# Kernel tuning notes

Measured on AMD Instinct MI355X. Metric: run time of the kernel, lower is better.

The kernel has to match this reference:

```python
import jax, jax.numpy as jnp
import numpy as np

N_MEL = 80; H = 512; HD = H // 2; R = 2; A = 128; NF = 32; K = 31
EMB = 512; ENC = 512; NSYM = 100


def _lstm_layer(x, lengths, Wih, Whh, b):
    # x: [B,T,D]; masked unidirectional LSTM (packed-sequence semantics:
    # state frozen and output zero past each sequence length).
    B, T, _ = x.shape
    Hh = Whh.shape[1]
    def step(carry, inp):
        h, c = carry
        xt, t = inp
        g = xt @ Wih.T + h @ Whh.T + b
        i, f, gg, o = jnp.split(g, 4, axis=-1)
        c_new = jax.nn.sigmoid(f) * c + jax.nn.sigmoid(i) * jnp.tanh(gg)
        h_new = jax.nn.sigmoid(o) * jnp.tanh(c_new)
        m = (t < lengths)[:, None]
        return (jnp.where(m, h_new, h), jnp.where(m, c_new, c)), jnp.where(m, h_new, 0.0)
    init = (jnp.zeros((B, Hh), x.dtype), jnp.zeros((B, Hh), x.dtype))
    _, ys = jax.lax.scan(step, init, (x.transpose(1, 0, 2), jnp.arange(T)))
    return ys.transpose(1, 0, 2)


def _bilstm(x, lengths, fw, bw):
    # bidirectional masked LSTM: backward dir runs on the sequence reversed
    # within its valid length (pack_padded_sequence semantics).
    T = x.shape[1]
    t = jnp.arange(T)
    idx = jnp.clip(lengths[:, None] - 1 - t[None, :], 0)
    x_rev = jnp.take_along_axis(x, idx[:, :, None], axis=1)
    out_f = _lstm_layer(x, lengths, *fw)
    out_r = _lstm_layer(x_rev, lengths, *bw)
    out_b = jnp.take_along_axis(out_r, idx[:, :, None], axis=1)
    out_b = jnp.where((t[None, :] < lengths[:, None])[:, :, None], out_b, 0.0)
    return jnp.concatenate([out_f, out_b], axis=-1)


def _forward(mel, mel_lengths, decoder_inputs, start_embedding,
             l1f_Wih, l1f_Whh, l1f_b, l1b_Wih, l1b_Whh, l1b_b,
             l2f_Wih, l2f_Whh, l2f_b, l2b_Wih, l2b_Whh, l2b_b,
             dec_Wih, dec_Whh, dec_b,
             q_W, m_W, loc_conv_W, loc_W, v_W,
             ph_W, ph_b, ps_W, ps_b):
    B = mel.shape[0]
    x = mel.transpose(0, 2, 1)                                   # [B,T,80]
    out1 = _bilstm(x, mel_lengths, (l1f_Wih, l1f_Whh, l1f_b), (l1b_Wih, l1b_Whh, l1b_b))
    out1 = out1.reshape(B, -1, H * R)                             # [B,T/R,H*R]
    mem_len = jnp.ceil(mel_lengths.astype(jnp.float32) / R).astype(jnp.int32)
    memory = _bilstm(out1, mem_len, (l2f_Wih, l2f_Whh, l2f_b), (l2b_Wih, l2b_Whh, l2b_b))  # [B,T',H]
    Tm = memory.shape[1]
    pad_mask = jnp.arange(Tm)[None, :] >= mem_len[:, None]        # True where padded
    processed_memory = memory @ m_W.T                             # [B,T',A]

    dec_seq = jnp.concatenate([start_embedding[None], decoder_inputs.transpose(2, 0, 1)], axis=0)  # [T+1,B,EMB]

    pad = (K - 1) // 2

    def dec_step(state, dinp):
        h, c, aw, awc, ctx = state
        cell_in = jnp.concatenate([dinp, ctx], axis=-1)
        g = cell_in @ dec_Wih.T + h @ dec_Whh.T + dec_b
        i, f, gg, o = jnp.split(g, 4, axis=-1)
        c = jax.nn.sigmoid(f) * c + jax.nn.sigmoid(i) * jnp.tanh(gg)
        h = jax.nn.sigmoid(o) * jnp.tanh(c)
        # location-sensitive attention
        aw_cat = jnp.stack([aw, awc], axis=1)                     # [B,2,T']
        loc = jax.lax.conv_general_dilated(aw_cat, loc_conv_W, (1,), [(pad, pad)],
                                           dimension_numbers=('NCH', 'OIH', 'NCH'))
        loc = loc.transpose(0, 2, 1) @ loc_W.T                    # [B,T',A]
        q = (h @ q_W.T)[:, None, :]                               # [B,1,A]
        e = jnp.tanh(q + loc + processed_memory) @ v_W.T          # [B,T',1]
        e = jnp.where(pad_mask, -1e9, e[..., 0])
        aw_new = jax.nn.softmax(e, axis=1)
        ctx_new = jnp.einsum('bt,btd->bd', aw_new, memory)
        awc_new = awc + aw_new
        hid = jax.nn.relu(jnp.concatenate([h, ctx_new], axis=-1) @ ph_W.T + ph_b)
        logit = hid @ ps_W.T + ps_b                               # dropout is identity in eval
        return (h, c, aw_new, awc_new, ctx_new), (hid, logit, aw_new)

    z = jnp.zeros((B, H), mel.dtype)
    init = (z, z, jnp.zeros((B, Tm), mel.dtype), jnp.zeros((B, Tm), mel.dtype), z)
    _, (hiddens, logits, aligns) = jax.lax.scan(dec_step, init, dec_seq)
    return (hiddens.transpose(1, 0, 2), logits.transpose(1, 0, 2), aligns.transpose(1, 0, 2))


def setup_inputs() -> dict:
    key = jax.random.key(0)
    ks = iter(jax.random.split(key, 40))
    B, T, TD = 32, 1600, 160
    s = 0.05
    def w(shape):
        return jax.random.normal(next(ks), shape, jnp.float32) * s
    mel_lengths = jax.random.randint(next(ks), (B,), T // 2, T + 1)
    mel_lengths = mel_lengths.at[0].set(T)
    return {
        'mel': jax.random.normal(next(ks), (B, N_MEL, T), jnp.float32),
        'mel_lengths': mel_lengths,
        'decoder_inputs': jax.random.normal(next(ks), (B, EMB, TD), jnp.float32),
        'start_embedding': jax.random.normal(next(ks), (B, EMB), jnp.float32),
        'l1f_Wih': w((4 * HD, N_MEL)), 'l1f_Whh': w((4 * HD, HD)), 'l1f_b': w((4 * HD,)),
        'l1b_Wih': w((4 * HD, N_MEL)), 'l1b_Whh': w((4 * HD, HD)), 'l1b_b': w((4 * HD,)),
        'l2f_Wih': w((4 * HD, H * R)), 'l2f_Whh': w((4 * HD, HD)), 'l2f_b': w((4 * HD,)),
        'l2b_Wih': w((4 * HD, H * R)), 'l2b_Whh': w((4 * HD, HD)), 'l2b_b': w((4 * HD,)),
        'dec_Wih': w((4 * H, EMB + H)), 'dec_Whh': w((4 * H, H)), 'dec_b': w((4 * H,)),
        'q_W': w((A, H)), 'm_W': w((A, H)), 'loc_conv_W': w((NF, 2, K)),
        'loc_W': w((A, NF)), 'v_W': w((1, A)),
        'ph_W': w((ENC, H + H)), 'ph_b': w((ENC,)),
        'ps_W': w((NSYM + 1, ENC)), 'ps_b': w((NSYM + 1,)),
    }


def reference(mel, mel_lengths, decoder_inputs, start_embedding,
              l1f_Wih, l1f_Whh, l1f_b, l1b_Wih, l1b_Whh, l1b_b,
              l2f_Wih, l2f_Whh, l2f_b, l2b_Wih, l2b_Whh, l2b_b,
              dec_Wih, dec_Whh, dec_b,
              q_W, m_W, loc_conv_W, loc_W, v_W,
              ph_W, ph_b, ps_W, ps_b):
    return _forward(mel, mel_lengths, decoder_inputs, start_embedding,
                    l1f_Wih, l1f_Whh, l1f_b, l1b_Wih, l1b_Whh, l1b_b,
                    l2f_Wih, l2f_Whh, l2f_b, l2b_Wih, l2b_Whh, l2b_b,
                    dec_Wih, dec_Whh, dec_b,
                    q_W, m_W, loc_conv_W, loc_W, v_W,
                    ph_W, ph_b, ps_W, ps_b)
```

## Files before the change

### kernel.cpp

```cpp
#include <hip/hip_runtime.h>
#include <hip/hip_bf16.h>

typedef __hip_bfloat16 bf16;
typedef __attribute__((ext_vector_type(8))) short short8v;
typedef __attribute__((ext_vector_type(4))) float float4v;
#define DEVINL __device__ __forceinline__

DEVINL float bfu2f(unsigned int u){ union{unsigned int u; float f;} c; c.u=u; return c.f; }
DEVINL float b2f(bf16 v){ return __bfloat162float(v); }
DEVINL bf16  f2b(float f){ return __float2bfloat16(f); }
DEVINL float sigf(float x){ return 1.f/(1.f+__expf(-x)); }
DEVINL float tanhfast(float x){
  float t=__expf(-2.f*fabsf(x));
  float r=(1.f-t)/(1.f+t);
  return copysignf(r,x);
}
DEVINL void hilo(float x, short& h, short& l){
  bf16 hb = __float2bfloat16(x);
  bf16 lb = __float2bfloat16(x - __bfloat162float(hb));
  h = *(short*)&hb; l = *(short*)&lb;
}
DEVINL void ld4(const bf16* __restrict__ p, float* d){
  uint2 v = *reinterpret_cast<const uint2*>(p);
  d[0]=bfu2f(v.x<<16); d[1]=bfu2f(v.x&0xffff0000u);
  d[2]=bfu2f(v.y<<16); d[3]=bfu2f(v.y&0xffff0000u);
}
DEVINL void ld4(const float* __restrict__ p, float* d){
  float4 v = *reinterpret_cast<const float4*>(p);
  d[0]=v.x; d[1]=v.y; d[2]=v.z; d[3]=v.w;
}
DEVINL void st1(bf16* p, float v){ *p = f2b(v); }
DEVINL void st1(float* p, float v){ *p = v; }

__global__ void k_zero_f(float* p, long n){
  long i=(long)blockIdx.x*256+threadIdx.x, st=(long)gridDim.x*256;
  for(;i<n;i+=st) p[i]=0.f;
}
__global__ void k_zero_b(bf16* p, long n){
  long i=(long)blockIdx.x*256+threadIdx.x, st=(long)gridDim.x*256;
  for(;i<n;i+=st) p[i]=f2b(0.f);
}
__global__ void k_xT(const float* __restrict__ mel, float* __restrict__ xT){
  int i = blockIdx.x*256+threadIdx.x; if(i>=51200*80) return;
  int m = i/80, d = i - m*80; int b = m/1600, t = m - b*1600;
  xT[i] = mel[((size_t)b*80 + d)*1600 + t];
}
__global__ void k_cvt(const float* __restrict__ W, bf16* __restrict__ o, int n){
  int i=blockIdx.x*256+threadIdx.x; if(i<n) o[i]=f2b(W[i]);
}
__global__ void k_cvt2(const float* __restrict__ W, bf16* __restrict__ hi,
                       bf16* __restrict__ lo, int n){
  int i=blockIdx.x*256+threadIdx.x; if(i>=n) return;
  short h,l; hilo(W[i], h, l);
  hi[i]=*(bf16*)&h; lo[i]=*(bf16*)&l;
}
__global__ void k_whh_il8(const float* __restrict__ W, bf16* __restrict__ il){
  int i = blockIdx.x*256+threadIdx.x; if(i>=262144) return;
  int kk = i&7; int j = (i>>3)&1023; int kc = i>>13;
  il[i] = f2b(W[j*256 + kc*8 + kk]);
}
__global__ void k_psW(const float* __restrict__ W, const float* __restrict__ bsrc,
                      float* __restrict__ Wp, float* __restrict__ bp){
  int i=blockIdx.x*256+threadIdx.x;
  if(i<128*512){ int n=i/512,k=i-n*512; Wp[i] = (n<101)? W[n*512+k] : 0.f; }
  else if(i<128*512+128){ int n=i-128*512; bp[n]=(n<101)? bsrc[n]:0.f; }
}
__global__ void k_dseq(const float* __restrict__ start, const float* __restrict__ dec_in,
                       float* __restrict__ dseq){
  int i=blockIdx.x*256+threadIdx.x; if(i>=5184*512) return;
  int r=i/512, e=i-r*512;
  float v=0.f;
  if (r<5152){ int s=r/32, b=r-s*32;
    v = (s==0)? start[b*512+e] : dec_in[(size_t)b*81920 + e*160 + (s-1)];
  }
  dseq[i]=v;
}

template<bool RELU, typename TA, typename TCO>
__global__ __launch_bounds__(256) void gemm64(
    const TA* __restrict__ A, int lda, int T, int TC, int t0,
    const int* __restrict__ lens, int lenDiv, int rev,
    const float* __restrict__ W, int ldw,
    const float* __restrict__ bias,
    TCO* __restrict__ C, int ldc, int K)
{
  __shared__ float As[16][64];
  __shared__ float Ws[16][64];
  const int tid = threadIdx.x;
  const int n0 = blockIdx.x*64, m0 = blockIdx.y*64;
  const int tx = tid & 15, ty = tid >> 4;
  const int r = tid >> 2, c4 = (tid & 3) * 4;
  const int m = m0 + r;
  size_t arow;
  if (lens){
    int b = m / TC, tc = m - b*TC, t = t0 + tc;
    if (rev){
      int L = lens[b]; if (lenDiv==2) L=(L+1)>>1;
      t = L-1-t; if (t<0) t=0;
    }
    arow = (size_t)b*T + t;
  } else arow = (size_t)m;
  float acc[4][4] = {{0.f}};
  for (int k0=0; k0<K; k0+=16){
    float av[4];
    ld4(A + arow*lda + k0 + c4, av);
    const float4 wv = *reinterpret_cast<const float4*>(&W[(size_t)(n0+r)*ldw + k0 + c4]);
    As[c4+0][r] = av[0]; As[c4+1][r] = av[1]; As[c4+2][r] = av[2]; As[c4+3][r] = av[3];
    Ws[c4+0][r] = wv.x; Ws[c4+1][r]=wv.y; Ws[c4+2][r]=wv.z; Ws[c4+3][r]=wv.w;
    __syncthreads();
    #pragma unroll
    for(int k=0;k<16;k++){
      const float4 a = *reinterpret_cast<const float4*>(&As[k][ty*4]);
      const float4 w = *reinterpret_cast<const float4*>(&Ws[k][tx*4]);
      acc[0][0] += a.x*w.x; acc[0][1] += a.x*w.y; acc[0][2] += a.x*w.z; acc[0][3] += a.x*w.w;
      acc[1][0] += a.y*w.x; acc[1][1] += a.y*w.y; acc[1][2] += a.y*w.z; acc[1][3] += a.y*w.w;
      acc[2][0] += a.z*w.x; acc[2][1] += a.z*w.y; acc[2][2] += a.z*w.z; acc[2][3] += a.z*w.w;
      acc[3][0] += a.w*w.x; acc[3][1] += a.w*w.y; acc[3][2] += a.w*w.z; acc[3][3] += a.w*w.w;
    }
    __syncthreads();
  }
  #pragma unroll
  for(int i=0;i<4;i++){
    const size_t row = (size_t)m0 + ty*4 + i;
    #pragma unroll
    for(int j=0;j<4;j++){
      const int col = n0 + tx*4 + j;
      float v = acc[i][j] + (bias ? bias[col] : 0.f);
      if (RELU) v = fmaxf(v, 0.f);
      st1(&C[row*ldc + col], v);
    }
  }
}

template<bool RELU, typename TCO>
__global__ __launch_bounds__(256) void gemmM(
    const bf16* __restrict__ A, int lda, int T, int TC, int t0,
    const int* __restrict__ lens, int lenDiv, int rev,
    const short* __restrict__ Whi, const short* __restrict__ Wlo, int ldw,
    const float* __restrict__ bias,
    TCO* __restrict__ C, int ldc, int K)
{
  __shared__ short As[128][40];
  __shared__ short Bs[2][128][40];
  const int tid = threadIdx.x;
  const int lane = tid & 63, wave = tid >> 6;
  const int wm = wave >> 1, wn = wave & 1;
  const int n0 = blockIdx.x*128, m0 = blockIdx.y*128;

  auto arow_of = [&](int m)->size_t{
    if (lens){
      int b = m / TC, tc = m - b*TC, t = t0 + tc;
      if (rev){ int L=lens[b]; if(lenDiv==2) L=(L+1)>>1; t=L-1-t; if(t<0)t=0; }
      return (size_t)b*T + t;
    }
    return (size_t)m;
  };

  float4v acc[4][4];
  #pragma unroll
  for (int i=0;i<4;++i)
    #pragma unroll
    for (int j=0;j<4;++j) acc[i][j] = (float4v){0.f,0.f,0.f,0.f};

  const int ar = tid>>2, akp = (tid&3)*8;
  const size_t arow0 = arow_of(m0 + ar), arow1 = arow_of(m0 + ar + 64);
  const short* Ash = (const short*)A;

  for (int k0=0; k0<K; k0+=32){
    *(short8v*)&As[ar][akp]    = *(const short8v*)(Ash + arow0*lda + k0 + akp);
    *(short8v*)&As[ar+64][akp] = *(const short8v*)(Ash + arow1*lda + k0 + akp);
    *(short8v*)&Bs[0][ar][akp]    = *(const short8v*)(Whi + (size_t)(n0+ar)*ldw + k0 + akp);
    *(short8v*)&Bs[0][ar+64][akp] = *(const short8v*)(Whi + (size_t)(n0+ar+64)*ldw + k0 + akp);
    *(short8v*)&Bs[1][ar][akp]    = *(const short8v*)(Wlo + (size_t)(n0+ar)*ldw + k0 + akp);
    *(short8v*)&Bs[1][ar+64][akp] = *(const short8v*)(Wlo + (size_t)(n0+ar+64)*ldw + k0 + akp);
    __syncthreads();
    const int l15 = lane & 15, kb8 = (lane>>4)*8;
    short8v a0[4], bh[4], bl[4];
    #pragma unroll
    for (int mt=0;mt<4;++mt) a0[mt] = *(const short8v*)&As[wm*64+mt*16+l15][kb8];
    #pragma unroll
    for (int nt=0;nt<4;++nt){
      bh[nt] = *(const short8v*)&Bs[0][wn*64+nt*16+l15][kb8];
      bl[nt] = *(const short8v*)&Bs[1][wn*64+nt*16+l15][kb8];
    }
    #pragma unroll
    for (int mt=0;mt<4;++mt)
      #pragma unroll
      for (int nt=0;nt<4;++nt){
        acc[mt][nt] = __builtin_amdgcn_mfma_f32_16x16x32_bf16(a0[mt], bh[nt], acc[mt][nt], 0,0,0);
        acc[mt][nt] = __builtin_amdgcn_mfma_f32_16x16x32_bf16(a0[mt], bl[nt], acc[mt][nt], 0,0,0);
      }
    __syncthreads();
  }
  const int l15 = lane & 15, rb = (lane>>4)*4;
  #pragma unroll
  for (int mt=0;mt<4;++mt){
    #pragma unroll
    for (int nt=0;nt<4;++nt){
      const int col = n0 + wn*64 + nt*16 + l15;
      const float bv = bias ? bias[col] : 0.f;
      #pragma unroll
      for (int i=0;i<4;++i){
        const size_t row = (size_t)m0 + wm*64 + mt*16 + rb + i;
        float v = acc[mt][nt][i] + bv;
        if (RELU) v = fmaxf(v, 0.f);
        st1(&C[row*ldc + col], v);
      }
    }
  }
}

__global__ __launch_bounds__(1024) void lstm8(
   const bf16* __restrict__ Pf, const bf16* __restrict__ Pb,
   const bf16* __restrict__ Whf, const bf16* __restrict__ Whb,
   const int* __restrict__ lens, int lenDiv, int t0, int TC,
   bf16* __restrict__ out, int T, float* __restrict__ hc)
{
  const int b = blockIdx.x, dir = blockIdx.y, j = threadIdx.x;
  int L = lens[b]; if (lenDiv==2) L = (L+1)>>1;
  const bf16* P  = (dir ? Pb : Pf) + (size_t)b*TC*1024;
  const bf16* wil = (dir ? Whb : Whf) + (size_t)j*8;
  float* hcp = hc + (size_t)(dir*32+b)*512;
  __shared__ float hs[256];
  __shared__ float gs[1024];
  if (j<256) hs[j] = hcp[j];
  float c = (j<256) ? hcp[256+j] : 0.f;
  __syncthreads();
  int tcEnd = L - t0; if (tcEnd > TC) tcEnd = TC;
  for (int tc=0; tc<tcEnd; ++tc){
    float acc = b2f(P[(size_t)tc*1024 + j]);
    #pragma unroll 8
    for (int kc=0; kc<32; ++kc){
      const uint4 wv = *reinterpret_cast<const uint4*>(wil + (size_t)kc*8192);
      const int k = kc*8;
      acc += bfu2f(wv.x<<16)*hs[k]   + bfu2f(wv.x&0xffff0000u)*hs[k+1]
           + bfu2f(wv.y<<16)*hs[k+2] + bfu2f(wv.y&0xffff0000u)*hs[k+3]
           + bfu2f(wv.z<<16)*hs[k+4] + bfu2f(wv.z&0xffff0000u)*hs[k+5]
           + bfu2f(wv.w<<16)*hs[k+6] + bfu2f(wv.w&0xffff0000u)*hs[k+7];
    }
    gs[j] = acc;
    __syncthreads();
    if (j<256){
      const float cn = sigf(gs[256+j])*c + sigf(gs[j])*tanhfast(gs[512+j]);
      const float hn = sigf(gs[768+j])*tanhfast(cn);
      c = cn;
      const int t = t0+tc;
      const int srow = dir ? (L-1-t) : t;
      out[((size_t)b*T + srow)*512 + dir*256 + j] = f2b(hn);
      hs[j] = hn;
    }
    __syncthreads();
  }
  if (j<256){ hcp[j]=hs[j]; hcp[256+j]=c; }
}

__global__ __launch_bounds__(256) void dec_g(
  const bf16* __restrict__ Pd, const float* __restrict__ Wih,
  const float* __restrict__ Whh, const float* __restrict__ h_state,
  const float* __restrict__ ctx_state, float* __restrict__ g_buf, int s)
{
  const int b = blockIdx.x, jt = blockIdx.y, tid = threadIdx.x;
  const int j = jt*256 + tid;
  __shared__ float cs[512], hs[512];
  cs[tid] = ctx_state[b*512+tid]; cs[256+tid] = ctx_state[b*512+256+tid];
  hs[tid] = h_state[b*512+tid];   hs[256+tid] = h_state[b*512+256+tid];
  __syncthreads();
  float acc = b2f(Pd[((size_t)(s*32+b))*2048 + j]);
  const float* wc = Wih + (size_t)j*1024 + 512;
  const float* wh = Whh + (size_t)j*512;
  for (int k=0;k<512;k+=4){
    const float4 cv = *(const float4*)&cs[k];
    const float4 hv = *(const float4*)&hs[k];
    const float4 a  = *(const float4*)&wc[k];
    const float4 b4 = *(const float4*)&wh[k];
    acc += a.x*cv.x + a.y*cv.y + a.z*cv.z + a.w*cv.w;
    acc += b4.x*hv.x + b4.y*hv.y + b4.z*hv.z + b4.w*hv.w;
  }
  g_buf[b*2048 + j] = acc;
}

__global__ __launch_bounds__(512) void dec_rest(
  const float* __restrict__ g_buf, const float* __restrict__ qW,
  const float* __restrict__ convW, const float* __restrict__ locW,
  const float* __restrict__ vW, const float* __restrict__ PM, const bf16* __restrict__ memB,
  const int* __restrict__ lens,
  float* __restrict__ h_state, float* __restrict__ c_state, float* __restrict__ ctx_state,
  float* __restrict__ aw_state, float* __restrict__ awc_state,
  float* __restrict__ hallctx, float* __restrict__ outA, int s)
{
  const int b = blockIdx.x, u = threadIdx.x;
  __shared__ float hsh[512], red[512], aw_s[800], q_s[128], v_s[128];
  __shared__ float convW_s[1984], locW_s[4096];
  for (int i=u; i<1984; i+=512) convW_s[i]=convW[i];
  for (int i=u; i<4096; i+=512) locW_s[i]=locW[i];
  if (u<128) v_s[u]=vW[u];
  {
    const float gi = g_buf[b*2048 + u],     gf = g_buf[b*2048+512+u];
    const float gg = g_buf[b*2048+1024+u],  go = g_buf[b*2048+1536+u];
    const float cn = sigf(gf)*c_state[b*512+u] + sigf(gi)*tanhfast(gg);
    const float hn = sigf(go)*tanhfast(cn);
    c_state[b*512+u]=cn; h_state[b*512+u]=hn; hsh[u]=hn;
    hallctx[((size_t)(s*32+b))*1024 + u] = hn;
  }
  __syncthreads();
  if (u<128){
    const float* wr = qW + u*512;
    float acc=0.f;
    for (int k=0;k<512;k+=4){
      const float4 w = *(const float4*)&wr[k];
      const float4 h = *(const float4*)&hsh[k];
      acc += w.x*h.x + w.y*h.y + w.z*h.z + w.w*h.w;
    }
    q_s[u]=acc;
  }
  __syncthreads();
  const int mlen = (lens[b]+1)>>1;
  float ex0=0.f, ex1=0.f;
  #pragma unroll
  for (int rep=0; rep<2; ++rep){
    const int t = u + rep*512;
    float ex = 0.f;
    if (t < 800 && t < mlen){
      float convf[32];
      #pragma unroll
      for (int f=0;f<32;++f) convf[f]=0.f;
      for (int k=0;k<31;++k){
        const int pos = t-15+k;
        const bool ok = (pos>=0 && pos<800);
        const float a0 = ok ? aw_state[b*800+pos] : 0.f;
        const float a1 = ok ? awc_state[b*800+pos] : 0.f;
        #pragma unroll
        for (int f=0;f<32;++f)
          convf[f] += convW_s[(f*2+0)*31+k]*a0 + convW_s[(f*2+1)*31+k]*a1;
      }
      const float* pm = PM + ((size_t)b*800 + t)*128;
      float e = 0.f;
      for (int a=0;a<128;++a){
        float loc = 0.f;
        #pragma unroll
        for (int f=0;f<32;++f) loc += convf[f]*locW_s[a*32+f];
        e += v_s[a]*tanhfast(q_s[a]+loc+pm[a]);
      }
      ex = __expf(e);
    }
    if (rep==0) ex0=ex; else ex1=ex;
  }
  red[u]=ex0+ex1; __syncthreads();
  for (int st=256; st>0; st>>=1){
    if (u<st) red[u]+=red[u+st];
    __syncthreads();
  }
  const float invZ = 1.f/red[0];
  {
    const float a0 = ex0*invZ;
    aw_s[u]=a0; aw_state[b*800+u]=a0; awc_state[b*800+u]+=a0;
    outA[((size_t)b*161+s)*800+u] = a0;
    const int t1=u+512;
    if (t1<800){
      const float a1 = ex1*invZ;
      aw_s[t1]=a1; aw_state[b*800+t1]=a1; awc_state[b*800+t1]+=a1;
      outA[((size_t)b*161+s)*800+t1] = a1;
    }
  }
  __syncthreads();
  float ctxa = 0.f;
  for (int t2=0;t2<800;++t2)
    ctxa += aw_s[t2]*b2f(memB[((size_t)b*800+t2)*512 + u]);
  ctx_state[b*512+u]=ctxa;
  hallctx[((size_t)(s*32+b))*1024 + 512 + u] = ctxa;
}

__global__ void k_scat_h(const float* __restrict__ hid, float* __restrict__ outH){
  int i=blockIdx.x*256+threadIdx.x; if(i>=5152*512) return;
  int r=i>>9, d=i&511; int s=r>>5, b=r&31;
  outH[((size_t)b*161+s)*512 + d] = hid[i];
}
__global__ void k_scat_l(const float* __restrict__ lg, float* __restrict__ outL){
  int i=blockIdx.x*256+threadIdx.x; if(i>=5152*101) return;
  int r=i/101, n=i-r*101; int s=r>>5, b=r&31;
  outL[((size_t)b*161+s)*101 + n] = lg[r*128+n];
}

extern "C" void kernel_launch(void* const* d_in, const int* in_sizes, int n_in,
                              void* d_out, int out_size, void* d_ws, size_t ws_size,
                              hipStream_t stream)
{
  const float* mel    = (const float*)d_in[0];
  const int*   lens   = (const int*)  d_in[1];
  const float* dec_in = (const float*)d_in[2];
  const float* start  = (const float*)d_in[3];
  const float* l1fWih = (const float*)d_in[4];
  const float* l1fWhh = (const float*)d_in[5];
  const float* l1fb   = (const float*)d_in[6];
  const float* l1bWih = (const float*)d_in[7];
  const float* l1bWhh = (const float*)d_in[8];
  const float* l1bb   = (const float*)d_in[9];
  const float* l2fWih = (const float*)d_in[10];
  const float* l2fWhh = (const float*)d_in[11];
  const float* l2fb   = (const float*)d_in[12];
  const float* l2bWih = (const float*)d_in[13];
  const float* l2bWhh = (const float*)d_in[14];
  const float* l2bb   = (const float*)d_in[15];
  const float* decWih = (const float*)d_in[16];
  const float* decWhh = (const float*)d_in[17];
  const float* decb   = (const float*)d_in[18];
  const float* qW     = (const float*)d_in[19];
  const float* mW     = (const float*)d_in[20];
  const float* convW  = (const float*)d_in[21];
  const float* locW   = (const float*)d_in[22];
  const float* vW     = (const float*)d_in[23];
  const float* phW    = (const float*)d_in[24];
  const float* phb    = (const float*)d_in[25];
  const float* psW    = (const float*)d_in[26];
  const float* psb    = (const float*)d_in[27];
  (void)in_sizes; (void)n_in; (void)out_size; (void)ws_size;

  char* wsp = (char*)d_ws;
  size_t off = 0;
  auto alloc = [&](size_t bytes)->char*{
    char* p = wsp + off; off += (bytes + 255) & ~(size_t)255; return p;
  };

  float* stateF   = (float*)alloc((size_t)100352*4);
  float* h_state  = stateF;
  float* c_state  = stateF + 16384;
  float* ctx_state= stateF + 32768;
  float* aw_state = stateF + 49152;
  float* awc_state= stateF + 74752;
  float* hc_enc   = (float*)alloc((size_t)32768*4);
  float* g_buf    = (float*)alloc((size_t)65536*4);
  float* psW_p    = (float*)alloc((size_t)65536*4);
  float* psb_p    = (float*)alloc((size_t)128*4);
  bf16*  whh1f    = (bf16*)alloc((size_t)262144*2);
  bf16*  whh1b    = (bf16*)alloc((size_t)262144*2);
  bf16*  whh2f    = (bf16*)alloc((size_t)262144*2);
  bf16*  whh2b    = (bf16*)alloc((size_t)262144*2);
  bf16*  w_m_h    = (bf16*)alloc((size_t)65536*2);
  bf16*  w_m_l    = (bf16*)alloc((size_t)65536*2);

  char* R_X = alloc((size_t)16384000);
  float* xT   = (float*)R_X;
  bf16*  w_l2f_h = (bf16*)R_X;
  bf16*  w_l2f_l = (bf16*)(R_X + 2097152);
  bf16*  w_l2b_h = (bf16*)(R_X + 4194304);
  bf16*  w_l2b_l = (bf16*)(R_X + 6291456);
  float* dseq = (float*)R_X;
  float* hid  = (float*)R_X;
  char* R_P = alloc((size_t)26214400);
  bf16* Pchf = (bf16*)R_P;
  bf16* Pchb = (bf16*)(R_P + 10485760);
  bf16* Pd   = (bf16*)R_P;
  float* logitb = (float*)R_P;
  char* R_O = alloc((size_t)52428800);
  bf16*  out1    = (bf16*)R_O;
  float* PM      = (float*)R_O;
  float* hallctx = (float*)(R_O + 13107200);
  char* R_M = alloc((size_t)26214400);
  bf16*  memB = (bf16*)R_M;

  float* outF = (float*)d_out;
  float* outH = outF;
  float* outL = outF + 2637824;
  float* outA = outF + 3158176;

  k_zero_f<<<392,256,0,stream>>>(stateF, 100352);
  k_zero_f<<<128,256,0,stream>>>(hc_enc, 32768);
  k_xT<<<16000,256,0,stream>>>(mel, xT);
  k_whh_il8<<<1024,256,0,stream>>>(l1fWhh, whh1f);
  k_whh_il8<<<1024,256,0,stream>>>(l1bWhh, whh1b);
  k_whh_il8<<<1024,256,0,stream>>>(l2fWhh, whh2f);
  k_whh_il8<<<1024,256,0,stream>>>(l2bWhh, whh2b);
  k_cvt2<<<256,256,0,stream>>>(mW, w_m_h, w_m_l, 65536);
  k_psW<<<257,256,0,stream>>>(psW, psb, psW_p, psb_p);
  k_zero_b<<<2048,256,0,stream>>>(out1, 26214400);
  k_zero_b<<<2048,256,0,stream>>>(memB, 13107200);

  for (int c=0;c<10;++c){
    const int t0 = c*160;
    gemm64<false,float,bf16><<<dim3(16,80),256,0,stream>>>(xT,80, 1600,160,t0, lens,1,0,
                                                l1fWih,80, l1fb, Pchf,1024, 80);
    gemm64<false,float,bf16><<<dim3(16,80),256,0,stream>>>(xT,80, 1600,160,t0, lens,1,1,
                                                l1bWih,80, l1bb, Pchb,1024, 80);
    lstm8<<<dim3(32,2),1024,0,stream>>>(Pchf,Pchb, whh1f,whh1b, lens,1, t0,160, out1, 1600, hc_enc);
  }

  k_cvt2<<<4096,256,0,stream>>>(l2fWih, w_l2f_h, w_l2f_l, 1048576);
  k_cvt2<<<4096,256,0,stream>>>(l2bWih, w_l2b_h, w_l2b_l, 1048576);

  k_zero_f<<<128,256,0,stream>>>(hc_enc, 32768);
  for (int c=0;c<5;++c){
    const int t0 = c*160;
    gemmM<false,bf16><<<dim3(8,40),256,0,stream>>>(out1,1024, 800,160,t0, lens,2,0,
        (const short*)w_l2f_h,(const short*)w_l2f_l,1024, l2fb, Pchf,1024, 1024);
    gemmM<false,bf16><<<dim3(8,40),256,0,stream>>>(out1,1024, 800,160,t0, lens,2,1,
        (const short*)w_l2b_h,(const short*)w_l2b_l,1024, l2bb, Pchb,1024, 1024);
    lstm8<<<dim3(32,2),1024,0,stream>>>(Pchf,Pchb, whh2f,whh2b, lens,2, t0,160, memB, 800, hc_enc);
  }

  k_dseq<<<10368,256,0,stream>>>(start, dec_in, dseq);
  gemmM<false,float><<<dim3(1,200),256,0,stream>>>(memB,512, 0,0,0, nullptr,0,0,
      (const short*)w_m_h,(const short*)w_m_l,512, (const float*)nullptr, PM,128, 512);
  k_zero_f<<<2048,256,0,stream>>>(hallctx, 5308416);
  gemm64<false,float,bf16><<<dim3(32,81),256,0,stream>>>(dseq,512, 0,0,0, nullptr,0,0,
                                                decWih,1024, decb, Pd,2048, 512);

  for (int s=0; s<161; ++s){
    dec_g<<<dim3(32,8),256,0,stream>>>(Pd, decWih, decWhh, h_state, ctx_state, g_buf, s);
    dec_rest<<<32,512,0,stream>>>(g_buf, qW, convW, locW, vW, PM, memB, lens,
                                  h_state, c_state, ctx_state, aw_state, awc_state,
                                  hallctx, outA, s);
  }

  gemm64<true ,float,float><<<dim3(8,81),256,0,stream>>>(hallctx,1024, 0,0,0, nullptr,0,0,
                                                phW,1024, phb, hid,512, 1024);
  gemm64<false,float,float><<<dim3(2,81),256,0,stream>>>(hid,512, 0,0,0, nullptr,0,0,
                                                psW_p,512, psb_p, logitb,128, 512);
  k_scat_h<<<10304,256,0,stream>>>(hid, outH);
  k_scat_l<<<2033,256,0,stream>>>(logitb, outL);
}
```

Before: 43.52 ms.

## Move decoder gate, layer-1 input and decoder input projections to MFMA split-bf16 GEMM

Replaces the per-step fp32 decoder gate kernel (dec_g) with the MFMA-based gemmM using hi/lo bf16 split weights. The concatenated [ctx,h] state is written as bf16 into a small buffer by dec_rest. The layer-1 input projection and the decoder input projection also move to gemmM, with inputs padded to 96 and stored as bf16. The aim is to replace the slow scalar fp32 matvecs inside the 161-step decoder loop and the SIMT GEMMs with matrix-core work. The cost is extra weight conversion kernels and some precision loss from rounding activations to bf16.

```diff
diff --git a/kernel.cpp b/kernel.cpp
--- a/kernel.cpp
+++ b/kernel.cpp
@@ -40,13 +40,18 @@
   long i=(long)blockIdx.x*256+threadIdx.x, st=(long)gridDim.x*256;
   for(;i<n;i+=st) p[i]=f2b(0.f);
 }
-__global__ void k_xT(const float* __restrict__ mel, float* __restrict__ xT){
-  int i = blockIdx.x*256+threadIdx.x; if(i>=51200*80) return;
-  int m = i/80, d = i - m*80; int b = m/1600, t = m - b*1600;
-  xT[i] = mel[((size_t)b*80 + d)*1600 + t];
-}
-__global__ void k_cvt(const float* __restrict__ W, bf16* __restrict__ o, int n){
-  int i=blockIdx.x*256+threadIdx.x; if(i<n) o[i]=f2b(W[i]);
+__global__ void k_xT96b(const float* __restrict__ mel, bf16* __restrict__ xT){
+  int i = blockIdx.x*256+threadIdx.x; if(i>=51200*96) return;
+  int m = i/96, d = i - m*96; int b = m/1600, t = m - b*1600;
+  xT[i] = f2b((d<80)? mel[((size_t)b*80 + d)*1600 + t] : 0.f);
+}
+__global__ void k_padW96b2(const float* __restrict__ W, bf16* __restrict__ hi,
+                           bf16* __restrict__ lo){
+  int i = blockIdx.x*256+threadIdx.x; if(i>=1024*96) return;
+  int j=i/96, d=i-j*96;
+  float x = (d<80)? W[j*80+d] : 0.f;
+  short h,l; hilo(x,h,l);
+  hi[i]=*(bf16*)&h; lo[i]=*(bf16*)&l;
 }
 __global__ void k_cvt2(const float* __restrict__ W, bf16* __restrict__ hi,
                        bf16* __restrict__ lo, int n){
@@ -65,15 +70,26 @@
   if(i<128*512){ int n=i/512,k=i-n*512; Wp[i] = (n<101)? W[n*512+k] : 0.f; }
   else if(i<128*512+128){ int n=i-128*512; bp[n]=(n<101)? bsrc[n]:0.f; }
 }
-__global__ void k_dseq(const float* __restrict__ start, const float* __restrict__ dec_in,
-                       float* __restrict__ dseq){
-  int i=blockIdx.x*256+threadIdx.x; if(i>=5184*512) return;
-  int r=i/512, e=i-r*512;
-  float v=0.f;
-  if (r<5152){ int s=r/32, b=r-s*32;
-    v = (s==0)? start[b*512+e] : dec_in[(size_t)b*81920 + e*160 + (s-1)];
-  }
-  dseq[i]=v;
+__global__ void k_dseqb(const float* __restrict__ start, const float* __restrict__ dec_in,
+                        bf16* __restrict__ dseq){
+  int i=blockIdx.x*256+threadIdx.x; if(i>=5152*512) return;
+  int r=i/512, e=i-r*512; int s=r/32, b=r-s*32;
+  dseq[i] = f2b((s==0)? start[b*512+e] : dec_in[(size_t)b*81920 + e*160 + (s-1)]);
+}
+__global__ void k_wpd(const float* __restrict__ Wih, bf16* __restrict__ hi,
+                      bf16* __restrict__ lo){
+  int i=blockIdx.x*256+threadIdx.x; if(i>=2048*512) return;
+  int j=i>>9, k=i&511;
+  short h,l; hilo(Wih[(size_t)j*1024 + k], h, l);
+  hi[i]=*(bf16*)&h; lo[i]=*(bf16*)&l;
+}
+__global__ void k_wdg(const float* __restrict__ Wih, const float* __restrict__ Whh,
+                      bf16* __restrict__ hi, bf16* __restrict__ lo){
+  int i=blockIdx.x*256+threadIdx.x; if(i>=2048*1024) return;
+  int j=i>>10, k=i&1023;
+  float x = (k<512)? Wih[(size_t)j*1024 + 512 + k] : Whh[(size_t)j*512 + (k-512)];
+  short h,l; hilo(x,h,l);
+  hi[i]=*(bf16*)&h; lo[i]=*(bf16*)&l;
 }
 
 template<bool RELU, typename TA, typename TCO>
@@ -254,39 +270,15 @@
   if (j<256){ hcp[j]=hs[j]; hcp[256+j]=c; }
 }
 
-__global__ __launch_bounds__(256) void dec_g(
-  const bf16* __restrict__ Pd, const float* __restrict__ Wih,
-  const float* __restrict__ Whh, const float* __restrict__ h_state,
-  const float* __restrict__ ctx_state, float* __restrict__ g_buf, int s)
-{
-  const int b = blockIdx.x, jt = blockIdx.y, tid = threadIdx.x;
-  const int j = jt*256 + tid;
-  __shared__ float cs[512], hs[512];
-  cs[tid] = ctx_state[b*512+tid]; cs[256+tid] = ctx_state[b*512+256+tid];
-  hs[tid] = h_state[b*512+tid];   hs[256+tid] = h_state[b*512+256+tid];
-  __syncthreads();
-  float acc = b2f(Pd[((size_t)(s*32+b))*2048 + j]);
-  const float* wc = Wih + (size_t)j*1024 + 512;
-  const float* wh = Whh + (size_t)j*512;
-  for (int k=0;k<512;k+=4){
-    const float4 cv = *(const float4*)&cs[k];
-    const float4 hv = *(const float4*)&hs[k];
-    const float4 a  = *(const float4*)&wc[k];
-    const float4 b4 = *(const float4*)&wh[k];
-    acc += a.x*cv.x + a.y*cv.y + a.z*cv.z + a.w*cv.w;
-    acc += b4.x*hv.x + b4.y*hv.y + b4.z*hv.z + b4.w*hv.w;
-  }
-  g_buf[b*2048 + j] = acc;
-}
-
 __global__ __launch_bounds__(512) void dec_rest(
-  const float* __restrict__ g_buf, const float* __restrict__ qW,
+  const float* __restrict__ g_buf, const bf16* __restrict__ Pd,
+  const float* __restrict__ qW,
   const float* __restrict__ convW, const float* __restrict__ locW,
   const float* __restrict__ vW, const float* __restrict__ PM, const bf16* __restrict__ memB,
   const int* __restrict__ lens,
   float* __restrict__ h_state, float* __restrict__ c_state, float* __restrict__ ctx_state,
   float* __restrict__ aw_state, float* __restrict__ awc_state,
-  float* __restrict__ hallctx, float* __restrict__ outA, int s)
+  float* __restrict__ hallctx, bf16* __restrict__ abuf, float* __restrict__ outA, int s)
 {
   const int b = blockIdx.x, u = threadIdx.x;
   __shared__ float hsh[512], red[512], aw_s[800], q_s[128], v_s[128];
@@ -295,12 +287,16 @@
   for (int i=u; i<4096; i+=512) locW_s[i]=locW[i];
   if (u<128) v_s[u]=vW[u];
   {
-    const float gi = g_buf[b*2048 + u],     gf = g_buf[b*2048+512+u];
-    const float gg = g_buf[b*2048+1024+u],  go = g_buf[b*2048+1536+u];
+    const bf16* pd = Pd + (size_t)(s*32+b)*2048;
+    const float gi = g_buf[b*2048 + u]      + b2f(pd[u]);
+    const float gf = g_buf[b*2048+512+u]    + b2f(pd[512+u]);
+    const float gg = g_buf[b*2048+1024+u]   + b2f(pd[1024+u]);
+    const float go = g_buf[b*2048+1536+u]   + b2f(pd[1536+u]);
     const float cn = sigf(gf)*c_state[b*512+u] + sigf(gi)*tanhfast(gg);
     const float hn = sigf(go)*tanhfast(cn);
     c_state[b*512+u]=cn; h_state[b*512+u]=hn; hsh[u]=hn;
     hallctx[((size_t)(s*32+b))*1024 + u] = hn;
+    abuf[b*1024 + 512 + u] = f2b(hn);
   }
   __syncthreads();
   if (u<128){
@@ -368,6 +364,7 @@
     ctxa += aw_s[t2]*b2f(memB[((size_t)b*800+t2)*512 + u]);
   ctx_state[b*512+u]=ctxa;
   hallctx[((size_t)(s*32+b))*1024 + 512 + u] = ctxa;
+  abuf[b*1024 + u] = f2b(ctxa);
 }
 
 __global__ void k_scat_h(const float* __restrict__ hid, float* __restrict__ outH){
@@ -428,7 +425,8 @@
   float* aw_state = stateF + 49152;
   float* awc_state= stateF + 74752;
   float* hc_enc   = (float*)alloc((size_t)32768*4);
-  float* g_buf    = (float*)alloc((size_t)65536*4);
+  float* g_buf    = (float*)alloc((size_t)262144*4);
+  bf16*  abuf     = (bf16*)alloc((size_t)131072*2);
   float* psW_p    = (float*)alloc((size_t)65536*4);
   float* psb_p    = (float*)alloc((size_t)128*4);
   bf16*  whh1f    = (bf16*)alloc((size_t)262144*2);
@@ -437,24 +435,32 @@
   bf16*  whh2b    = (bf16*)alloc((size_t)262144*2);
   bf16*  w_m_h    = (bf16*)alloc((size_t)65536*2);
   bf16*  w_m_l    = (bf16*)alloc((size_t)65536*2);
-
-  char* R_X = alloc((size_t)16384000);
-  float* xT   = (float*)R_X;
+  bf16*  w_l1f_h  = (bf16*)alloc((size_t)98304*2);
+  bf16*  w_l1f_l  = (bf16*)alloc((size_t)98304*2);
+  bf16*  w_l1b_h  = (bf16*)alloc((size_t)98304*2);
+  bf16*  w_l1b_l  = (bf16*)alloc((size_t)98304*2);
+
+  char* R_X = alloc((size_t)10747904);
+  bf16*  xTb   = (bf16*)R_X;
   bf16*  w_l2f_h = (bf16*)R_X;
   bf16*  w_l2f_l = (bf16*)(R_X + 2097152);
   bf16*  w_l2b_h = (bf16*)(R_X + 4194304);
   bf16*  w_l2b_l = (bf16*)(R_X + 6291456);
-  float* dseq = (float*)R_X;
+  bf16*  dseqB = (bf16*)R_X;
+  bf16*  w_pd_h = (bf16*)(R_X + 5505024);
+  bf16*  w_pd_l = (bf16*)(R_X + 7602176);
   float* hid  = (float*)R_X;
   char* R_P = alloc((size_t)26214400);
   bf16* Pchf = (bf16*)R_P;
   bf16* Pchb = (bf16*)(R_P + 10485760);
   bf16* Pd   = (bf16*)R_P;
-  float* logitb = (float*)R_P;
+  float* logitb = (float*)(R_P + 21495808);
   char* R_O = alloc((size_t)52428800);
   bf16*  out1    = (bf16*)R_O;
   float* PM      = (float*)R_O;
   float* hallctx = (float*)(R_O + 13107200);
+  bf16*  w_dg_h  = (bf16*)(R_O + 34340864);
+  bf16*  w_dg_l  = (bf16*)(R_O + 38535168);
   char* R_M = alloc((size_t)26214400);
   bf16*  memB = (bf16*)R_M;
 
@@ -465,7 +471,10 @@
 
   k_zero_f<<<392,256,0,stream>>>(stateF, 100352);
   k_zero_f<<<128,256,0,stream>>>(hc_enc, 32768);
-  k_xT<<<16000,256,0,stream>>>(mel, xT);
+  k_zero_b<<<512,256,0,stream>>>(abuf, 131072);
+  k_xT96b<<<19200,256,0,stream>>>(mel, xTb);
+  k_padW96b2<<<384,256,0,stream>>>(l1fWih, w_l1f_h, w_l1f_l);
+  k_padW96b2<<<384,256,0,stream>>>(l1bWih, w_l1b_h, w_l1b_l);
   k_whh_il8<<<1024,256,0,stream>>>(l1fWhh, whh1f);
   k_whh_il8<<<1024,256,0,stream>>>(l1bWhh, whh1b);
   k_whh_il8<<<1024,256,0,stream>>>(l2fWhh, whh2f);
@@ -477,10 +486,10 @@
 
   for (int c=0;c<10;++c){
     const int t0 = c*160;
-    gemm64<false,float,bf16><<<dim3(16,80),256,0,stream>>>(xT,80, 1600,160,t0, lens,1,0,
-                                                l1fWih,80, l1fb, Pchf,1024, 80);
-    gemm64<false,float,bf16><<<dim3(16,80),256,0,stream>>>(xT,80, 1600,160,t0, lens,1,1,
-                                                l1bWih,80, l1bb, Pchb,1024, 80);
+    gemmM<false,bf16><<<dim3(8,40),256,0,stream>>>(xTb,96, 1600,160,t0, lens,1,0,
+        (const short*)w_l1f_h,(const short*)w_l1f_l,96, l1fb, Pchf,1024, 96);
+    gemmM<false,bf16><<<dim3(8,40),256,0,stream>>>(xTb,96, 1600,160,t0, lens,1,1,
+        (const short*)w_l1b_h,(const short*)w_l1b_l,96, l1bb, Pchb,1024, 96);
     lstm8<<<dim3(32,2),1024,0,stream>>>(Pchf,Pchb, whh1f,whh1b, lens,1, t0,160, out1, 1600, hc_enc);
   }
 
@@ -497,18 +506,22 @@
     lstm8<<<dim3(32,2),1024,0,stream>>>(Pchf,Pchb, whh2f,whh2b, lens,2, t0,160, memB, 800, hc_enc);
   }
 
-  k_dseq<<<10368,256,0,stream>>>(start, dec_in, dseq);
   gemmM<false,float><<<dim3(1,200),256,0,stream>>>(memB,512, 0,0,0, nullptr,0,0,
       (const short*)w_m_h,(const short*)w_m_l,512, (const float*)nullptr, PM,128, 512);
+  k_zero_b<<<2048,256,0,stream>>>(dseqB, 2686976);
+  k_dseqb<<<10304,256,0,stream>>>(start, dec_in, dseqB);
+  k_wpd<<<4096,256,0,stream>>>(decWih, w_pd_h, w_pd_l);
+  gemmM<false,bf16><<<dim3(16,41),256,0,stream>>>(dseqB,512, 0,0,0, nullptr,0,0,
+      (const short*)w_pd_h,(const short*)w_pd_l,512, decb, Pd,2048, 512);
   k_zero_f<<<2048,256,0,stream>>>(hallctx, 5308416);
-  gemm64<false,float,bf16><<<dim3(32,81),256,0,stream>>>(dseq,512, 0,0,0, nullptr,0,0,
-                                                decWih,1024, decb, Pd,2048, 512);
+  k_wdg<<<8192,256,0,stream>>>(decWih, decWhh, w_dg_h, w_dg_l);
 
   for (int s=0; s<161; ++s){
-    dec_g<<<dim3(32,8),256,0,stream>>>(Pd, decWih, decWhh, h_state, ctx_state, g_buf, s);
-    dec_rest<<<32,512,0,stream>>>(g_buf, qW, convW, locW, vW, PM, memB, lens,
+    gemmM<false,float><<<dim3(16,1),256,0,stream>>>(abuf,1024, 0,0,0, nullptr,0,0,
+        (const short*)w_dg_h,(const short*)w_dg_l,1024, (const float*)nullptr, g_buf,2048, 1024);
+    dec_rest<<<32,512,0,stream>>>(g_buf, Pd, qW, convW, locW, vW, PM, memB, lens,
                                   h_state, c_state, ctx_state, aw_state, awc_state,
-                                  hallctx, outA, s);
+                                  hallctx, abuf, outA, s);
   }
 
   gemm64<true ,float,float><<<dim3(8,81),256,0,stream>>>(hallctx,1024, 0,0,0, nullptr,0,0,
```

Measured after the change: 46.15 ms. 6.0% more time.
